# Optimization experiments

Hardware: AMD Instinct MI355X
Metric: run time of the kernel (lower is better)

The kernel has to match this reference:

```python
import jax, jax.numpy as jnp
import numpy as np
from jax import lax

USER_NUM = 60000
ITEM_NUM = 40000
N_NODES = USER_NUM + ITEM_NUM
EMB = 64
NNZ = 3200000
N_LAYERS = 3
ALPHA = 0.1


def setup_inputs() -> dict:
    key = jax.random.key(0)
    k1, k2, k3, k4, k5 = jax.random.split(key, 5)
    rows = jax.random.randint(k1, (NNZ,), 0, N_NODES, dtype=jnp.int32)
    cols = jax.random.randint(k2, (NNZ,), 0, N_NODES, dtype=jnp.int32)
    # normalized adjacency values are small positives
    vals = jax.random.uniform(k3, (NNZ,), dtype=jnp.float32) * 0.05
    user_emb = jax.random.normal(k4, (USER_NUM, EMB), dtype=jnp.float32) * 0.1
    item_emb = jax.random.normal(k5, (ITEM_NUM, EMB), dtype=jnp.float32) * 0.1
    return {"rows": rows, "cols": cols, "vals": vals,
            "user_emb": user_emb, "item_emb": item_emb}


def reference(rows, cols, vals, user_emb, item_emb):
    # ego = cat(user, item); e_out starts at zeros (first forward call).
    ego = jnp.concatenate([user_emb, item_emb], axis=0)  # [N, d]
    e0 = jnp.zeros_like(ego)

    def step(e, _):
        # torch.sparse.mm(A, e.clone().detach()) -> SpMM with stop_gradient,
        # matching the original's detach of the propagated state.
        gathered = vals[:, None] * lax.stop_gradient(e)[cols]  # [nnz, d]
        msg = jax.ops.segment_sum(gathered, rows, num_segments=N_NODES)
        e_new = (1.0 - ALPHA) * msg + ego
        return e_new, None

    e_out, _ = lax.scan(step, e0, None, length=N_LAYERS)
    return e_out[:USER_NUM], e_out[USER_NUM:]
```

## Files before the change

### kernel.cpp

```cpp
#include <hip/hip_runtime.h>
#include <hip/hip_fp16.h>


#define USER_NUM 60000
#define ITEM_NUM 40000
#define N_NODES  100000
#define EMB      64
#define NNZ      3200000
#define OMA       0.9f
#define BR       128
#define NB       782
#define TILE     4096
#define CAPB     4480

typedef float f32x4 __attribute__((ext_vector_type(4)));

__global__ __launch_bounds__(256) void conv_init(const float* __restrict__ ue,
                                                 const float* __restrict__ ie,
                                                 __half* __restrict__ dst,
                                                 int* __restrict__ bcursor) {
    int t = blockIdx.x * 256 + threadIdx.x;
    if (t < NB) bcursor[t] = t * CAPB;
    const int total8 = N_NODES * EMB / 8;
    if (t >= total8) return;
    size_t f0 = (size_t)t * 8;
    const size_t usz = (size_t)USER_NUM * EMB;
    const float4* s4 = (f0 < usz) ? (const float4*)(ue + f0)
                                  : (const float4*)(ie + (f0 - usz));
    float4 x = s4[0], y = s4[1];
    union { float4 f4; __half2 h2[4]; } o;
    o.h2[0] = __floats2half2_rn(x.x, x.y);
    o.h2[1] = __floats2half2_rn(x.z, x.w);
    o.h2[2] = __floats2half2_rn(y.x, y.y);
    o.h2[3] = __floats2half2_rn(y.z, y.w);
    ((float4*)dst)[t] = o.f4;
}

__global__ __launch_bounds__(512) void bucket_scatter(const int* __restrict__ rows,
                                                      const int* __restrict__ cols,
                                                      const float* __restrict__ vals,
                                                      int* __restrict__ bcursor,
                                                      int2* __restrict__ ebuf) {
    __shared__ int bins[NB + 1];
    __shared__ int lcur[NB];
    __shared__ int wsum[8];
    __shared__ int2 stage[TILE];
    __shared__ unsigned short sbk[TILE];
    int t = threadIdx.x;
    int lane = t & 63, w = t >> 6;
    for (int b = t; b <= NB; b += 512) bins[b] = 0;
    __syncthreads();

    int e0 = blockIdx.x * TILE;
    int mybk[8], mypk[8];
    float myv[8];
#pragma unroll
    for (int j = 0; j < 8; ++j) {
        int i = e0 + t + 512 * j;
        mybk[j] = -1;
        if (i < NNZ) {
            int r = rows[i], c = cols[i];
            myv[j]  = vals[i] * OMA;
            mybk[j] = r >> 7;
            mypk[j] = c | ((r & 127) << 17);
            atomicAdd(&bins[mybk[j]], 1);
        }
    }
    __syncthreads();

    int b0 = t * 2;
    int r0 = (b0     < NB) ? bins[b0]     : 0;
    int r1 = (b0 + 1 < NB) ? bins[b0 + 1] : 0;
    int s = r0 + r1;
    int incl = s;
#pragma unroll
    for (int off = 1; off < 64; off <<= 1) {
        int v = __shfl_up(incl, off, 64);
        if (lane >= off) incl += v;
    }
    if (lane == 63) wsum[w] = incl;
    __syncthreads();
    int prefix = 0;
#pragma unroll
    for (int i = 0; i < 8; ++i) if (i < w) prefix += wsum[i];
    int excl = prefix + incl - s;
    if (b0     < NB) { bins[b0]     = excl; lcur[b0]     = excl; excl += r0; }
    if (b0 + 1 < NB) { bins[b0 + 1] = excl; lcur[b0 + 1] = excl; }
    if (t == 511) bins[NB] = prefix + incl;
    __syncthreads();

#pragma unroll
    for (int j = 0; j < 8; ++j) {
        if (mybk[j] >= 0) {
            int p = atomicAdd(&lcur[mybk[j]], 1);
            stage[p] = make_int2(mypk[j], __float_as_int(myv[j]));
            sbk[p] = (unsigned short)mybk[j];
        }
    }
    __syncthreads();

    for (int b = t; b < NB; b += 512) {
        int st = bins[b], en = bins[b + 1];
        int cnt = en - st;
        if (cnt > 0) lcur[b] = atomicAdd(&bcursor[b], cnt) - st;
    }
    __syncthreads();

    int total = bins[NB];
    for (int i = t; i < total; i += 512) {
        int bk = sbk[i];
        ebuf[(size_t)(lcur[bk] + i)] = stage[i];
    }
}

__global__ __launch_bounds__(512) void sort_spmm1(const int* __restrict__ bcursor,
                                                  int2* __restrict__ ebuf,
                                                  int* __restrict__ row_start,
                                                  int* __restrict__ row_end,
                                                  const __half* __restrict__ ego_h,
                                                  const float* __restrict__ ue,
                                                  const float* __restrict__ ie,
                                                  __half* __restrict__ e2h) {
    __shared__ int2 stage[CAPB];
    __shared__ int rhist[BR], rofs[BR], rcur[BR];
    int bk = blockIdx.x, t = threadIdx.x;
    int s = bk * CAPB;
    int cnt = min(bcursor[bk] - s, CAPB);

    if (t < BR) rhist[t] = 0;
    __syncthreads();
    for (int i = t; i < cnt; i += 512) {
        int2 v = ebuf[(size_t)(s + i)];
        stage[i] = v;
        atomicAdd(&rhist[(v.x >> 17) & 127], 1);
    }
    __syncthreads();
    if (t < 64) {
        int h0 = rhist[2 * t], h1 = rhist[2 * t + 1];
        int pair = h0 + h1;
        int incl = pair;
#pragma unroll
        for (int off = 1; off < 64; off <<= 1) {
            int v = __shfl_up(incl, off, 64);
            if (t >= off) incl += v;
        }
        int base = incl - pair;
        rofs[2 * t]     = base;      rcur[2 * t]     = base;
        rofs[2 * t + 1] = base + h0; rcur[2 * t + 1] = base + h0;
    }
    __syncthreads();
    if (t < BR) {
        int r = (bk << 7) + t;
        if (r < N_NODES) {
            row_start[r] = s + rofs[t];
            row_end[r]   = s + rofs[t] + rhist[t];
        }
    }
    for (int i = t; i < cnt; i += 512) {
        int2 v = stage[i];
        int p = atomicAdd(&rcur[(v.x >> 17) & 127], 1);
        ebuf[(size_t)(s + p)] = v;
    }
    __syncthreads();

    int lane  = t & 15;
    int qbase = (t & 63) & ~15;
    int g = t >> 4;
    const float2* srcv = (const float2*)ego_h;
#pragma unroll
    for (int rr = 0; rr < 4; ++rr) {
        int rl = (g << 2) | rr;
        int r  = (bk << 7) + rl;
        if (r >= N_NODES) break;
        const float* egop = (r < USER_NUM) ? (ue + (size_t)r * EMB)
                                           : (ie + (size_t)(r - USER_NUM) * EMB);
        float4 acc = ((const float4*)egop)[lane];
        int ss = s + rofs[rl];
        int ee = ss + rhist[rl];
        int2 cv = (ss + lane < ee) ? ebuf[(size_t)(ss + lane)] : make_int2(0, 0);
        for (int k = ss; k < ee; k += 16) {
            int idxn = k + 16 + lane;
            int2 nv = (idxn < ee) ? ebuf[(size_t)idxn] : make_int2(0, 0);
#pragma unroll
            for (int j = 0; j < 16; ++j) {
                int   cj = __shfl(cv.x, qbase + j, 64) & 0x1FFFF;
                float vj = __int_as_float(__shfl(cv.y, qbase + j, 64));
                union { float2 f2; __half2 h2[2]; } u;
                u.f2 = srcv[(size_t)cj * 16 + lane];
                float2 a = __half22float2(u.h2[0]);
                float2 b = __half22float2(u.h2[1]);
                acc.x += vj * a.x; acc.y += vj * a.y;
                acc.z += vj * b.x; acc.w += vj * b.y;
            }
            cv = nv;
        }
        union { float2 f2; __half2 h2[2]; } o;
        o.h2[0] = __floats2half2_rn(acc.x, acc.y);
        o.h2[1] = __floats2half2_rn(acc.z, acc.w);
        ((float2*)e2h)[(size_t)r * 16 + lane] = o.f2;
    }
}

__global__ __launch_bounds__(256) void spmm2(const int* __restrict__ row_start,
                                             const int* __restrict__ row_end,
                                             const int2* __restrict__ colval,
                                             const __half* __restrict__ src,
                                             const float* __restrict__ ue,
                                             const float* __restrict__ ie,
                                             float* __restrict__ outb) {
    int tid = blockIdx.x * 256 + threadIdx.x;
    int r = tid >> 4;
    if (r >= N_NODES) return;
    int lane  = threadIdx.x & 15;
    int qbase = (threadIdx.x & 63) & ~15;

    const float* egop = (r < USER_NUM) ? (ue + (size_t)r * EMB)
                                       : (ie + (size_t)(r - USER_NUM) * EMB);
    float4 acc = ((const float4*)egop)[lane];
    const float2* srcv = (const float2*)src;
    int s = row_start[r], e = row_end[r];

    int2 cv = (s + lane < e) ? colval[(size_t)(s + lane)] : make_int2(0, 0);
    for (int k = s; k < e; k += 16) {
        int idxn = k + 16 + lane;
        int2 nv = (idxn < e) ? colval[(size_t)idxn] : make_int2(0, 0);
#pragma unroll
        for (int j = 0; j < 16; ++j) {
            int   cj = __shfl(cv.x, qbase + j, 64) & 0x1FFFF;
            float vj = __int_as_float(__shfl(cv.y, qbase + j, 64));
            union { float2 f2; __half2 h2[2]; } u;
            u.f2 = srcv[(size_t)cj * 16 + lane];
            float2 a = __half22float2(u.h2[0]);
            float2 b = __half22float2(u.h2[1]);
            acc.x += vj * a.x; acc.y += vj * a.y;
            acc.z += vj * b.x; acc.w += vj * b.y;
        }
        cv = nv;
    }
    f32x4 av = { acc.x, acc.y, acc.z, acc.w };
    __builtin_nontemporal_store(av, &((f32x4*)outb)[(size_t)r * 16 + lane]);
}

extern "C" void kernel_launch(void* const* d_in, const int* in_sizes, int n_in,
                              void* d_out, int out_size, void* d_ws, size_t ws_size,
                              hipStream_t stream) {
    const int*   rows = (const int*)d_in[0];
    const int*   cols = (const int*)d_in[1];
    const float* vals = (const float*)d_in[2];
    const float* ue   = (const float*)d_in[3];
    const float* ie   = (const float*)d_in[4];
    float* out = (float*)d_out;

    char* ws = (char*)d_ws;
    __half* ego_h    = (__half*)ws;
    __half* e2h      = (__half*)(ws + 12800000);
    int2*   ebuf     = (int2*)(ws + 25600000);
    int*    row_s    = (int*)(ws + 53626880);
    int*    row_e    = (int*)(ws + 54026880);
    int*    bcursor  = (int*)(ws + 54426880);

    const int convBlocks = (N_NODES * EMB / 8 + 255) / 256;
    conv_init<<<convBlocks, 256, 0, stream>>>(ue, ie, ego_h, bcursor);

    const int tiles = (NNZ + TILE - 1) / TILE;
    bucket_scatter<<<tiles, 512, 0, stream>>>(rows, cols, vals, bcursor, ebuf);
    sort_spmm1<<<NB, 512, 0, stream>>>(bcursor, ebuf, row_s, row_e, ego_h, ue, ie, e2h);

    const int spmmBlocks = (N_NODES * 16 + 255) / 256;
    spmm2<<<spmmBlocks, 256, 0, stream>>>(row_s, row_e, ebuf, e2h, ue, ie, out);
}
```

Baseline: 279.5 us.

## Fuse fp16 conversion into bucket scatter and sort SpMM1 entries in LDS

The separate conversion kernel is removed. Its fp32-to-fp16 embedding conversion now runs at the start of bucket_scatter, and bcursor is zeroed with a memset so it holds a relative count instead of an absolute offset. sort_spmm1 keeps the bucket's edges in registers, sorts them by row into LDS, and reads them from LDS during the first SpMM instead of re-reading global memory. spmm2 loads the column and value stream with nontemporal 64-bit loads. The aim is to save a kernel launch and global round trips, at the cost of more registers in sort_spmm1. There is also an ordering risk: sort_spmm1 reads ego_h written by other blocks of the previous kernel, which is safe because the launches are stream-ordered.

```diff
diff --git a/kernel.cpp b/kernel.cpp
--- a/kernel.cpp
+++ b/kernel.cpp
@@ -12,33 +12,16 @@
 #define NB       782
 #define TILE     4096
 #define CAPB     4480
+#define EPT      9
 
 typedef float f32x4 __attribute__((ext_vector_type(4)));
-
-__global__ __launch_bounds__(256) void conv_init(const float* __restrict__ ue,
-                                                 const float* __restrict__ ie,
-                                                 __half* __restrict__ dst,
-                                                 int* __restrict__ bcursor) {
-    int t = blockIdx.x * 256 + threadIdx.x;
-    if (t < NB) bcursor[t] = t * CAPB;
-    const int total8 = N_NODES * EMB / 8;
-    if (t >= total8) return;
-    size_t f0 = (size_t)t * 8;
-    const size_t usz = (size_t)USER_NUM * EMB;
-    const float4* s4 = (f0 < usz) ? (const float4*)(ue + f0)
-                                  : (const float4*)(ie + (f0 - usz));
-    float4 x = s4[0], y = s4[1];
-    union { float4 f4; __half2 h2[4]; } o;
-    o.h2[0] = __floats2half2_rn(x.x, x.y);
-    o.h2[1] = __floats2half2_rn(x.z, x.w);
-    o.h2[2] = __floats2half2_rn(y.x, y.y);
-    o.h2[3] = __floats2half2_rn(y.z, y.w);
-    ((float4*)dst)[t] = o.f4;
-}
 
 __global__ __launch_bounds__(512) void bucket_scatter(const int* __restrict__ rows,
                                                       const int* __restrict__ cols,
                                                       const float* __restrict__ vals,
+                                                      const float* __restrict__ ue,
+                                                      const float* __restrict__ ie,
+                                                      __half* __restrict__ ego_h,
                                                       int* __restrict__ bcursor,
                                                       int2* __restrict__ ebuf) {
     __shared__ int bins[NB + 1];
@@ -48,6 +31,29 @@
     __shared__ unsigned short sbk[TILE];
     int t = threadIdx.x;
     int lane = t & 63, w = t >> 6;
+
+    {
+        const int total8 = N_NODES * EMB / 8;
+        const size_t usz = (size_t)USER_NUM * EMB;
+        int u0 = blockIdx.x * 1024;
+#pragma unroll
+        for (int q = 0; q < 2; ++q) {
+            int u = u0 + t + 512 * q;
+            if (u < total8) {
+                size_t f0 = (size_t)u * 8;
+                const float4* s4 = (f0 < usz) ? (const float4*)(ue + f0)
+                                              : (const float4*)(ie + (f0 - usz));
+                float4 x = s4[0], y = s4[1];
+                union { float4 f4; __half2 h2[4]; } o;
+                o.h2[0] = __floats2half2_rn(x.x, x.y);
+                o.h2[1] = __floats2half2_rn(x.z, x.w);
+                o.h2[2] = __floats2half2_rn(y.x, y.y);
+                o.h2[3] = __floats2half2_rn(y.z, y.w);
+                ((float4*)ego_h)[u] = o.f4;
+            }
+        }
+    }
+
     for (int b = t; b <= NB; b += 512) bins[b] = 0;
     __syncthreads();
 
@@ -101,8 +107,8 @@
 
     for (int b = t; b < NB; b += 512) {
         int st = bins[b], en = bins[b + 1];
-        int cnt = en - st;
-        if (cnt > 0) lcur[b] = atomicAdd(&bcursor[b], cnt) - st;
+        int c = en - st;
+        if (c > 0) lcur[b] = b * CAPB + atomicAdd(&bcursor[b], c) - st;
     }
     __syncthreads();
 
@@ -125,14 +131,21 @@
     __shared__ int rhist[BR], rofs[BR], rcur[BR];
     int bk = blockIdx.x, t = threadIdx.x;
     int s = bk * CAPB;
-    int cnt = min(bcursor[bk] - s, CAPB);
+    int cnt = min(bcursor[bk], CAPB);
 
     if (t < BR) rhist[t] = 0;
     __syncthreads();
-    for (int i = t; i < cnt; i += 512) {
-        int2 v = ebuf[(size_t)(s + i)];
-        stage[i] = v;
-        atomicAdd(&rhist[(v.x >> 17) & 127], 1);
+
+    int2 ev[EPT]; int erow[EPT];
+#pragma unroll
+    for (int j = 0; j < EPT; ++j) {
+        int i = t + 512 * j;
+        erow[j] = -1;
+        if (i < cnt) {
+            ev[j] = ebuf[(size_t)(s + i)];
+            erow[j] = (ev[j].x >> 17) & 127;
+            atomicAdd(&rhist[erow[j]], 1);
+        }
     }
     __syncthreads();
     if (t < 64) {
@@ -156,12 +169,15 @@
             row_end[r]   = s + rofs[t] + rhist[t];
         }
     }
-    for (int i = t; i < cnt; i += 512) {
-        int2 v = stage[i];
-        int p = atomicAdd(&rcur[(v.x >> 17) & 127], 1);
-        ebuf[(size_t)(s + p)] = v;
-    }
-    __syncthreads();
+#pragma unroll
+    for (int j = 0; j < EPT; ++j) {
+        if (erow[j] >= 0) {
+            int p = atomicAdd(&rcur[erow[j]], 1);
+            stage[p] = ev[j];
+        }
+    }
+    __syncthreads();
+    for (int i = t; i < cnt; i += 512) ebuf[(size_t)(s + i)] = stage[i];
 
     int lane  = t & 15;
     int qbase = (t & 63) & ~15;
@@ -175,12 +191,11 @@
         const float* egop = (r < USER_NUM) ? (ue + (size_t)r * EMB)
                                            : (ie + (size_t)(r - USER_NUM) * EMB);
         float4 acc = ((const float4*)egop)[lane];
-        int ss = s + rofs[rl];
+        int ss = rofs[rl];
         int ee = ss + rhist[rl];
-        int2 cv = (ss + lane < ee) ? ebuf[(size_t)(ss + lane)] : make_int2(0, 0);
         for (int k = ss; k < ee; k += 16) {
-            int idxn = k + 16 + lane;
-            int2 nv = (idxn < ee) ? ebuf[(size_t)idxn] : make_int2(0, 0);
+            int idx = k + lane;
+            int2 cv = (idx < ee) ? stage[idx] : make_int2(0, 0);
 #pragma unroll
             for (int j = 0; j < 16; ++j) {
                 int   cj = __shfl(cv.x, qbase + j, 64) & 0x1FFFF;
@@ -192,7 +207,6 @@
                 acc.x += vj * a.x; acc.y += vj * a.y;
                 acc.z += vj * b.x; acc.w += vj * b.y;
             }
-            cv = nv;
         }
         union { float2 f2; __half2 h2[2]; } o;
         o.h2[0] = __floats2half2_rn(acc.x, acc.y);
@@ -218,16 +232,20 @@
                                        : (ie + (size_t)(r - USER_NUM) * EMB);
     float4 acc = ((const float4*)egop)[lane];
     const float2* srcv = (const float2*)src;
+    const unsigned long long* cv8 = (const unsigned long long*)colval;
     int s = row_start[r], e = row_end[r];
 
-    int2 cv = (s + lane < e) ? colval[(size_t)(s + lane)] : make_int2(0, 0);
+    unsigned long long cv = 0;
+    if (s + lane < e) cv = __builtin_nontemporal_load(&cv8[(size_t)(s + lane)]);
     for (int k = s; k < e; k += 16) {
         int idxn = k + 16 + lane;
-        int2 nv = (idxn < e) ? colval[(size_t)idxn] : make_int2(0, 0);
+        unsigned long long nv = 0;
+        if (idxn < e) nv = __builtin_nontemporal_load(&cv8[(size_t)idxn]);
+        int cx = (int)(cv & 0xFFFFFFFFull), cy = (int)(cv >> 32);
 #pragma unroll
         for (int j = 0; j < 16; ++j) {
-            int   cj = __shfl(cv.x, qbase + j, 64) & 0x1FFFF;
-            float vj = __int_as_float(__shfl(cv.y, qbase + j, 64));
+            int   cj = __shfl(cx, qbase + j, 64) & 0x1FFFF;
+            float vj = __int_as_float(__shfl(cy, qbase + j, 64));
             union { float2 f2; __half2 h2[2]; } u;
             u.f2 = srcv[(size_t)cj * 16 + lane];
             float2 a = __half22float2(u.h2[0]);
@@ -259,11 +277,11 @@
     int*    row_e    = (int*)(ws + 54026880);
     int*    bcursor  = (int*)(ws + 54426880);
 
-    const int convBlocks = (N_NODES * EMB / 8 + 255) / 256;
-    conv_init<<<convBlocks, 256, 0, stream>>>(ue, ie, ego_h, bcursor);
+    hipMemsetAsync(bcursor, 0, NB * sizeof(int), stream);
 
     const int tiles = (NNZ + TILE - 1) / TILE;
-    bucket_scatter<<<tiles, 512, 0, stream>>>(rows, cols, vals, bcursor, ebuf);
+    bucket_scatter<<<tiles, 512, 0, stream>>>(rows, cols, vals, ue, ie, ego_h,
+                                              bcursor, ebuf);
     sort_spmm1<<<NB, 512, 0, stream>>>(bcursor, ebuf, row_s, row_e, ego_h, ue, ie, e2h);
 
     const int spmmBlocks = (N_NODES * 16 + 255) / 256;
```

Result: faster. 264.3 us (-5.4%).
